# Kernel tuning notes

Hardware: AMD Instinct MI355X
Metric: run time of the kernel (lower is better)

## Reference

```python
import jax, jax.numpy as jnp
import numpy as np

N = 100000   # nodes
E = 3200000  # edges
F = 128      # in = hidden = out channels
V = 8        # virtual nodes
L = 3        # conv layers
EPS = 1e-5


def setup_inputs() -> dict:
    key = jax.random.key(0)
    ks = jax.random.split(key, 16)
    rn = lambda k, s, sc=0.05: jax.random.normal(k, s, jnp.float32) * sc
    return {
        "x": rn(ks[0], (N, F), 1.0),
        "edge_index": jax.random.randint(ks[1], (2, E), 0, N, jnp.int32),
        "vn_mask": jax.random.randint(ks[2], (V, N), 0, 2, jnp.int32).astype(bool),
        "Wc": rn(ks[3], (L, F, F)),
        "bc": rn(ks[4], (L, F)),
        "bn_g": jnp.ones((L, F), jnp.float32),
        "bn_b": jnp.zeros((L, F), jnp.float32),
        "vn_embed": rn(ks[5], (V, F)),
        "mlp_W1": rn(ks[6], (L - 1, V, F, 2 * F)),
        "mlp_b1": rn(ks[7], (L - 1, V, 2 * F)),
        "ln1_g": jnp.ones((L - 1, V, 2 * F), jnp.float32),
        "ln1_b": jnp.zeros((L - 1, V, 2 * F), jnp.float32),
        "mlp_W2": rn(ks[8], (L - 1, V, 2 * F, F)),
        "mlp_b2": rn(ks[9], (L - 1, V, F)),
        "ln2_g": jnp.ones((L - 1, V, F), jnp.float32),
        "ln2_b": jnp.zeros((L - 1, V, F), jnp.float32),
    }


def _ln(h, g, b):
    m = h.mean(-1, keepdims=True)
    v = ((h - m) ** 2).mean(-1, keepdims=True)
    return (h - m) * jax.lax.rsqrt(v + EPS) * g + b


def _bn(h, g, b):  # training-mode batch stats over nodes (dropout p=0)
    m = h.mean(0)
    v = ((h - m) ** 2).mean(0)
    return (h - m) * jax.lax.rsqrt(v + EPS) * g + b


def reference(x, edge_index, vn_mask, Wc, bc, bn_g, bn_b, vn_embed,
              mlp_W1, mlp_b1, ln1_g, ln1_b, mlp_W2, mlp_b2, ln2_g, ln2_b):
    src, dst = edge_index[0], edge_index[1]
    loops = jnp.arange(N, dtype=src.dtype)
    src_f = jnp.concatenate([src, loops])   # GCN adds self-loops
    dst_f = jnp.concatenate([dst, loops])
    deg = jax.ops.segment_sum(jnp.ones(src_f.shape[0], x.dtype), dst_f, num_segments=N)
    dinv = jnp.where(deg > 0, jax.lax.rsqrt(deg), 0.0)
    norm = dinv[src_f] * dinv[dst_f]        # sym-normalized edge weights

    def gcn(h, W, b):  # PyG GCNConv: linear -> normalized scatter-sum -> bias
        hl = h @ W
        out = jax.ops.segment_sum(hl[src_f] * norm[:, None], dst_f, num_segments=N)
        return out + b

    maskf = vn_mask.astype(x.dtype)  # [V, N]
    vn = vn_embed                    # [V, F]
    embs = [x]
    for layer in range(L):
        h = embs[layer] + vn.sum(0, keepdims=True)       # aggregation='sum'
        h = gcn(h, Wc[layer], bc[layer])
        h = _bn(h, bn_g[layer], bn_b[layer])
        if layer != L - 1:
            h = jax.nn.relu(h)
        embs.append(h)
        if layer < L - 1:
            pooled = maskf @ embs[layer]                 # per-VN global_add_pool
            tmp = pooled + vn
            h1 = jax.nn.relu(jnp.einsum('vf,vfh->vh', tmp, mlp_W1[layer]) + mlp_b1[layer])
            h1 = _ln(h1, ln1_g[layer], ln1_b[layer])
            h2 = jax.nn.relu(jnp.einsum('vh,vhf->vf', h1, mlp_W2[layer]) + mlp_b2[layer])
            vn = _ln(h2, ln2_g[layer], ln2_b[layer])
    return embs[-1]  # JK='last'
```

## Files before the change

kernel.cpp:

```cpp
#include <hip/hip_runtime.h>
#include <hip/hip_bf16.h>
#include <hip/hip_fp16.h>

#define NN 100000
#define EE 3200000
#define FF 128
#define F2 256
#define VV 8
#define LL 3
#define EPSV 1e-5f
#define NB 98

static inline int idiv(int a, int b){ return (a + b - 1) / b; }

__global__ void k_deg(const int* __restrict__ dst, int* __restrict__ edeg){
  int stride = gridDim.x * 256;
  for (int e = blockIdx.x * 256 + threadIdx.x; e < EE; e += stride)
    atomicAdd(&edeg[dst[e]], 1);
}

__global__ void k_scanA(const int* __restrict__ edeg, int* __restrict__ offs,
                        int* __restrict__ bsum, float* __restrict__ dinv){
  __shared__ int s[1024];
  int t = threadIdx.x;
  int i = blockIdx.x * 1024 + t;
  int v = (i < NN) ? edeg[i] : 0;
  if (i < NN) dinv[i] = rsqrtf((float)(v + 1));
  int x = v;
  s[t] = x; __syncthreads();
  for (int d = 1; d < 1024; d <<= 1){
    int y = (t >= d) ? s[t - d] : 0;
    __syncthreads();
    x += y; s[t] = x;
    __syncthreads();
  }
  if (i < NN) offs[i] = x - v;
  if (t == 1023) bsum[blockIdx.x] = x;
}

__global__ void k_scanB(int* __restrict__ bsum){
  __shared__ int s[128];
  int t = threadIdx.x;
  s[t] = (t < NB) ? bsum[t] : 0;
  __syncthreads();
  if (t == 0){
    int run = 0;
    for (int k = 0; k < NB; ++k){ int tmp = s[k]; s[k] = run; run += tmp; }
  }
  __syncthreads();
  if (t < NB) bsum[t] = s[t];
}

__global__ void k_scanC(int* __restrict__ offs, const int* __restrict__ bsum,
                        int* __restrict__ cursor){
  int i = blockIdx.x * 256 + threadIdx.x;
  if (i < NN){
    int o = offs[i] + bsum[i >> 10];
    offs[i] = o;
    cursor[i] = o;
  }
  if (i == 0) offs[NN] = EE;
}

__global__ void k_scatter(const int* __restrict__ src, const int* __restrict__ dst,
                          int* __restrict__ cursor, int* __restrict__ ssorted){
  int stride = gridDim.x * 256;
  for (int e = blockIdx.x * 256 + threadIdx.x; e < EE; e += stride){
    int d = dst[e];
    int pos = atomicAdd(&cursor[d], 1);
    ssorted[pos] = src[e];
  }
}

__global__ void k_maskdetect(const unsigned char* __restrict__ m, int* __restrict__ flag){
  int any = 0;
  for (int t = threadIdx.x; t < 4096; t += 256)
    if ((t & 3) && m[t]) any = 1;
  if (any) atomicOr(flag, 1);
}

__launch_bounds__(256)
__global__ void k_matmul(const float* __restrict__ in, const float* __restrict__ W,
                         const float* __restrict__ vn, const float* __restrict__ dinv,
                         uint2* __restrict__ hlb){
  __shared__ float Ws[FF * FF];
  __shared__ float As[8 * FF];
  __shared__ float vs[FF];
  __shared__ float rv[FF];
  int tid = threadIdx.x;
  for (int t = tid; t < FF * FF; t += 256) Ws[t] = W[t];
  if (tid < FF){
    float s = 0.f;
    for (int v = 0; v < VV; ++v) s += vn[v * FF + tid];
    vs[tid] = s;
  }
  __syncthreads();
  if (tid < FF){
    float a = 0.f;
    for (int k = 0; k < FF; ++k) a += vs[k] * Ws[k * FF + tid];
    rv[tid] = a;
  }
  __syncthreads();
  int row = tid >> 5;
  int col = (tid & 31) * 4;
  float4 rvv = *(const float4*)&rv[col];
  for (int base = blockIdx.x * 8; base < NN; base += gridDim.x * 8){
    for (int t = tid; t < 8 * FF; t += 256)
      As[t] = in[(base + (t >> 7)) * FF + (t & 127)];
    __syncthreads();
    float4 acc = rvv;
    #pragma unroll 8
    for (int k = 0; k < FF; ++k){
      float a = As[row * FF + k];
      float4 wv = *(const float4*)&Ws[k * FF + col];
      acc.x += a * wv.x; acc.y += a * wv.y; acc.z += a * wv.z; acc.w += a * wv.w;
    }
    float d = dinv[base + row];
    __half2 h01 = __floats2half2_rn(acc.x * d, acc.y * d);
    __half2 h23 = __floats2half2_rn(acc.z * d, acc.w * d);
    uint2 pk;
    pk.x = *reinterpret_cast<unsigned int*>(&h01);
    pk.y = *reinterpret_cast<unsigned int*>(&h23);
    hlb[(size_t)(base + row) * 32 + (tid & 31)] = pk;
    __syncthreads();
  }
}

__launch_bounds__(256)
__global__ void k_gather(const unsigned int* __restrict__ hlb, const float* __restrict__ dinv,
                         const int* __restrict__ offs, const int* __restrict__ ssorted,
                         float2* __restrict__ agg2, float* __restrict__ stats){
  int tid = threadIdx.x;
  int lane = tid & 63;
  int wid = (blockIdx.x * 256 + tid) >> 6;
  int nw = (gridDim.x * 256) >> 6;
  float s0 = 0.f, s1 = 0.f, q0 = 0.f, q1 = 0.f;
  for (int n = wid; n < NN; n += nw){
    int off0 = offs[n], off1 = offs[n + 1];
    unsigned int ps = hlb[(size_t)n * 64 + lane];
    float2 acc = __half22float2(*reinterpret_cast<__half2*>(&ps));
    #pragma unroll 4
    for (int e = off0; e < off1; ++e){
      unsigned int p = hlb[(size_t)ssorted[e] * 64 + lane];
      float2 f = __half22float2(*reinterpret_cast<__half2*>(&p));
      acc.x += f.x; acc.y += f.y;
    }
    float dv = dinv[n];
    float v0 = acc.x * dv, v1 = acc.y * dv;
    agg2[(size_t)n * 64 + lane] = make_float2(v0, v1);
    s0 += v0; s1 += v1; q0 += v0 * v0; q1 += v1 * v1;
  }
  __shared__ float4 red[256];
  red[tid] = make_float4(s0, s1, q0, q1);
  __syncthreads();
  if (tid < 64){
    float4 a = red[tid], b = red[tid + 64], c = red[tid + 128], d = red[tid + 192];
    a.x += b.x + c.x + d.x; a.y += b.y + c.y + d.y;
    a.z += b.z + c.z + d.z; a.w += b.w + c.w + d.w;
    atomicAdd(&stats[2 * tid], a.x);
    atomicAdd(&stats[2 * tid + 1], a.y);
    atomicAdd(&stats[FF + 2 * tid], a.z);
    atomicAdd(&stats[FF + 2 * tid + 1], a.w);
  }
}

__launch_bounds__(256)
__global__ void k_bnapply(float4* __restrict__ h, const float* __restrict__ stats,
                          const float* __restrict__ g, const float* __restrict__ b,
                          int relu){
  __shared__ float ss[2 * FF];
  int tid = threadIdx.x;
  if (tid < FF){
    float mean = stats[tid] * (1.0f / NN);
    float var  = stats[FF + tid] * (1.0f / NN) - mean * mean;
    float sc = rsqrtf(var + EPSV) * g[tid];
    ss[tid] = sc;
    ss[FF + tid] = b[tid] - mean * sc;
  }
  __syncthreads();
  int n4 = NN * FF / 4;
  int stride = gridDim.x * 256;
  for (int i = blockIdx.x * 256 + tid; i < n4; i += stride){
    int c = (i & 31) * 4;
    float4 v = h[i];
    float4 sc = *(const float4*)&ss[c];
    float4 sh = *(const float4*)&ss[FF + c];
    v.x = v.x * sc.x + sh.x;
    v.y = v.y * sc.y + sh.y;
    v.z = v.z * sc.z + sh.z;
    v.w = v.w * sc.w + sh.w;
    if (relu){
      v.x = fmaxf(v.x, 0.f); v.y = fmaxf(v.y, 0.f);
      v.z = fmaxf(v.z, 0.f); v.w = fmaxf(v.w, 0.f);
    }
    h[i] = v;
  }
}

__global__ void k_pool(const float* __restrict__ emb, const unsigned char* __restrict__ m8,
                       const int* __restrict__ m32, const int* __restrict__ flag,
                       float* __restrict__ pooled){
  int isb = *flag;
  int tid = blockIdx.x * 256 + threadIdx.x;
  int j = tid & 127;
  int r = tid >> 7;
  int rs = (gridDim.x * 256) >> 7;
  float acc[VV];
  #pragma unroll
  for (int v = 0; v < VV; ++v) acc[v] = 0.f;
  for (; r < NN; r += rs){
    float xv = emb[r * FF + j];
    #pragma unroll
    for (int v = 0; v < VV; ++v){
      int mv = isb ? (int)m8[v * NN + r] : m32[v * NN + r];
      if (mv) acc[v] += xv;
    }
  }
  #pragma unroll
  for (int v = 0; v < VV; ++v) atomicAdd(&pooled[v * FF + j], acc[v]);
}

__device__ __forceinline__ float blockSum(float x, float* red, int tid){
  red[tid] = x; __syncthreads();
  #pragma unroll
  for (int s = 128; s >= 1; s >>= 1){
    if (tid < s) red[tid] += red[tid + s];
    __syncthreads();
  }
  float r = red[0];
  __syncthreads();
  return r;
}

__launch_bounds__(256)
__global__ void k_vnmlp(const float* __restrict__ pooled, const float* __restrict__ vnin,
                        const float* __restrict__ W1, const float* __restrict__ b1,
                        const float* __restrict__ g1, const float* __restrict__ bb1,
                        const float* __restrict__ W2, const float* __restrict__ b2,
                        const float* __restrict__ g2, const float* __restrict__ bb2,
                        float* __restrict__ vnout){
  int v = blockIdx.x;
  int tid = threadIdx.x;
  __shared__ float tmp_s[FF];
  __shared__ float h1_s[F2];
  __shared__ float red[256];
  if (tid < FF) tmp_s[tid] = pooled[v * FF + tid] + vnin[v * FF + tid];
  __syncthreads();
  const float* W1v = W1 + (size_t)v * FF * F2;
  float acc = b1[v * F2 + tid];
  for (int k = 0; k < FF; ++k) acc += tmp_s[k] * W1v[k * F2 + tid];
  acc = fmaxf(acc, 0.f);
  float sum = blockSum(acc, red, tid);
  float sq  = blockSum(acc * acc, red, tid);
  float mean = sum * (1.f / F2);
  float var  = sq * (1.f / F2) - mean * mean;
  float y = (acc - mean) * rsqrtf(var + EPSV) * g1[v * F2 + tid] + bb1[v * F2 + tid];
  h1_s[tid] = y;
  __syncthreads();
  const float* W2v = W2 + (size_t)v * F2 * FF;
  float h2 = 0.f;
  if (tid < FF){
    float a2 = b2[v * FF + tid];
    for (int k = 0; k < F2; ++k) a2 += h1_s[k] * W2v[k * FF + tid];
    h2 = fmaxf(a2, 0.f);
  }
  float sum2 = blockSum((tid < FF) ? h2 : 0.f, red, tid);
  float sq2  = blockSum((tid < FF) ? h2 * h2 : 0.f, red, tid);
  float mean2 = sum2 * (1.f / FF);
  float var2  = sq2 * (1.f / FF) - mean2 * mean2;
  if (tid < FF)
    vnout[v * FF + tid] = (h2 - mean2) * rsqrtf(var2 + EPSV) * g2[v * FF + tid]
                          + bb2[v * FF + tid];
}

extern "C" void kernel_launch(void* const* d_in, const int* in_sizes, int n_in,
                              void* d_out, int out_size, void* d_ws, size_t ws_size,
                              hipStream_t stream){
  const float* x        = (const float*)d_in[0];
  const int*   ei       = (const int*)d_in[1];
  const unsigned char* vmask8 = (const unsigned char*)d_in[2];
  const int*   vmask32  = (const int*)d_in[2];
  const float* Wc       = (const float*)d_in[3];
  const float* bn_g     = (const float*)d_in[5];
  const float* bn_b     = (const float*)d_in[6];
  const float* vn_embed = (const float*)d_in[7];
  const float* mlp_W1   = (const float*)d_in[8];
  const float* mlp_b1   = (const float*)d_in[9];
  const float* ln1_g    = (const float*)d_in[10];
  const float* ln1_b    = (const float*)d_in[11];
  const float* mlp_W2   = (const float*)d_in[12];
  const float* mlp_b2   = (const float*)d_in[13];
  const float* ln2_g    = (const float*)d_in[14];
  const float* ln2_b    = (const float*)d_in[15];
  float* out = (float*)d_out;

  unsigned int* hlb = (unsigned int*)d_ws;
  float* bufB    = (float*)(hlb + (size_t)NN * 64);
  int*   ssorted = (int*)(bufB + (size_t)NN * FF);
  int*   offs    = ssorted + EE;
  int*   cursor  = offs + NN + 1;
  int*   edeg    = cursor + NN;
  int*   bsum    = edeg + NN;
  float* dinv    = (float*)(bsum + 128);
  float* stats   = dinv + NN;
  float* pooled  = stats + 2 * FF;
  float* vnA     = pooled + VV * FF;
  float* vnB     = vnA + VV * FF;
  int*   mflag   = (int*)(vnB + VV * FF);

  const int* esrc = ei;
  const int* edst = ei + EE;

  hipMemsetAsync(edeg, 0, NN * sizeof(int), stream);
  k_deg<<<1024, 256, 0, stream>>>(edst, edeg);
  k_scanA<<<NB, 1024, 0, stream>>>(edeg, offs, bsum, dinv);
  k_scanB<<<1, 128, 0, stream>>>(bsum);
  k_scanC<<<idiv(NN, 256), 256, 0, stream>>>(offs, bsum, cursor);
  k_scatter<<<2048, 256, 0, stream>>>(esrc, edst, cursor, ssorted);

  hipMemsetAsync(mflag, 0, sizeof(int), stream);
  k_maskdetect<<<1, 256, 0, stream>>>(vmask8, mflag);

  const float* vncur = vn_embed;
  const float* embin = x;
  float* vnbufs[2] = {vnA, vnB};

  for (int l = 0; l < LL; ++l){
    float* agg = (l == 0) ? bufB : out;
    const float* Wl = Wc + (size_t)l * FF * FF;

    k_matmul<<<2048, 256, 0, stream>>>(embin, Wl, vncur, dinv, (uint2*)hlb);

    if (l < LL - 1){
      hipMemsetAsync(pooled, 0, VV * FF * sizeof(float), stream);
      k_pool<<<1024, 256, 0, stream>>>(embin, vmask8, vmask32, mflag, pooled);
    }

    hipMemsetAsync(stats, 0, 2 * FF * sizeof(float), stream);
    k_gather<<<2048, 256, 0, stream>>>(hlb, dinv, offs, ssorted, (float2*)agg, stats);
    k_bnapply<<<1024, 256, 0, stream>>>((float4*)agg, stats,
                                        bn_g + l * FF, bn_b + l * FF, (l < LL - 1) ? 1 : 0);

    if (l < LL - 1){
      k_vnmlp<<<VV, 256, 0, stream>>>(pooled, vncur,
          mlp_W1 + (size_t)l * VV * FF * F2, mlp_b1 + (size_t)l * VV * F2,
          ln1_g + (size_t)l * VV * F2, ln1_b + (size_t)l * VV * F2,
          mlp_W2 + (size_t)l * VV * F2 * FF, mlp_b2 + (size_t)l * VV * FF,
          ln2_g + (size_t)l * VV * FF, ln2_b + (size_t)l * VV * FF,
          vnbufs[l]);
      vncur = vnbufs[l];
      embin = agg;
    }
  }
}
```

Measured before the change: 1.741 ms.

## Fold BN+ReLU into next layer loads and two-pass bucketed CSR build

The batch-norm scale/shift and ReLU are no longer applied in a separate in-place pass for the first two layers. A tiny kernel computes the per-channel scale and shift, and the next layer's matmul and pool kernels apply them while loading their inputs. The edge scatter is split into a coarse bucket pass keyed by dst>>5, which packs the dst low bits with src, and a per-bucket placement pass, to improve locality of the atomic cursor updates and writes. The gather unroll is also raised; this adds an extra pass over the edges and reuses the hlb buffer as scratch for binning.

```diff
diff --git a/kernel.cpp b/kernel.cpp
--- a/kernel.cpp
+++ b/kernel.cpp
@@ -10,6 +10,10 @@
 #define LL 3
 #define EPSV 1e-5f
 #define NB 98
+#define BSH 5
+#define NBKT 3125
+#define SRCBITS 17
+#define SRCMASK 0x1FFFF
 
 static inline int idiv(int a, int b){ return (a + b - 1) / b; }
 
@@ -62,13 +66,31 @@
   if (i == 0) offs[NN] = EE;
 }
 
-__global__ void k_scatter(const int* __restrict__ src, const int* __restrict__ dst,
-                          int* __restrict__ cursor, int* __restrict__ ssorted){
+__global__ void k_binit(const int* __restrict__ offs, int* __restrict__ bktcur){
+  int b = blockIdx.x * 256 + threadIdx.x;
+  if (b < NBKT) bktcur[b] = offs[b << BSH];
+}
+
+__global__ void k_bin(const int* __restrict__ src, const int* __restrict__ dst,
+                      int* __restrict__ bktcur, unsigned int* __restrict__ binned){
   int stride = gridDim.x * 256;
   for (int e = blockIdx.x * 256 + threadIdx.x; e < EE; e += stride){
     int d = dst[e];
+    int pos = atomicAdd(&bktcur[d >> BSH], 1);
+    binned[pos] = ((unsigned int)(d & 31) << SRCBITS) | (unsigned int)src[e];
+  }
+}
+
+__global__ void k_place(const unsigned int* __restrict__ binned, const int* __restrict__ offs,
+                        int* __restrict__ cursor, int* __restrict__ ssorted){
+  int b = blockIdx.x;
+  int e0 = offs[b << BSH];
+  int e1 = offs[(b + 1) << BSH];
+  for (int e = e0 + threadIdx.x; e < e1; e += 256){
+    unsigned int v = binned[e];
+    int d = (b << BSH) | (int)(v >> SRCBITS);
     int pos = atomicAdd(&cursor[d], 1);
-    ssorted[pos] = src[e];
+    ssorted[pos] = (int)(v & SRCMASK);
   }
 }
 
@@ -82,17 +104,21 @@
 __launch_bounds__(256)
 __global__ void k_matmul(const float* __restrict__ in, const float* __restrict__ W,
                          const float* __restrict__ vn, const float* __restrict__ dinv,
+                         const float* __restrict__ ss, int hasbn,
                          uint2* __restrict__ hlb){
   __shared__ float Ws[FF * FF];
   __shared__ float As[8 * FF];
   __shared__ float vs[FF];
   __shared__ float rv[FF];
+  __shared__ float scs[FF], shs[FF];
   int tid = threadIdx.x;
   for (int t = tid; t < FF * FF; t += 256) Ws[t] = W[t];
   if (tid < FF){
     float s = 0.f;
     for (int v = 0; v < VV; ++v) s += vn[v * FF + tid];
     vs[tid] = s;
+    scs[tid] = hasbn ? ss[tid] : 1.0f;
+    shs[tid] = hasbn ? ss[FF + tid] : 0.0f;
   }
   __syncthreads();
   if (tid < FF){
@@ -105,8 +131,17 @@
   int col = (tid & 31) * 4;
   float4 rvv = *(const float4*)&rv[col];
   for (int base = blockIdx.x * 8; base < NN; base += gridDim.x * 8){
-    for (int t = tid; t < 8 * FF; t += 256)
-      As[t] = in[(base + (t >> 7)) * FF + (t & 127)];
+    if (hasbn){
+      for (int t = tid; t < 8 * FF; t += 256){
+        int c = t & 127;
+        float v = in[(base + (t >> 7)) * FF + c];
+        v = fmaf(v, scs[c], shs[c]);
+        As[t] = fmaxf(v, 0.f);
+      }
+    } else {
+      for (int t = tid; t < 8 * FF; t += 256)
+        As[t] = in[(base + (t >> 7)) * FF + (t & 127)];
+    }
     __syncthreads();
     float4 acc = rvv;
     #pragma unroll 8
@@ -139,7 +174,7 @@
     int off0 = offs[n], off1 = offs[n + 1];
     unsigned int ps = hlb[(size_t)n * 64 + lane];
     float2 acc = __half22float2(*reinterpret_cast<__half2*>(&ps));
-    #pragma unroll 4
+    #pragma unroll 8
     for (int e = off0; e < off1; ++e){
       unsigned int p = hlb[(size_t)ssorted[e] * 64 + lane];
       float2 f = __half22float2(*reinterpret_cast<__half2*>(&p));
@@ -164,10 +199,19 @@
   }
 }
 
+__global__ void k_bnfin(const float* __restrict__ stats, const float* __restrict__ g,
+                        const float* __restrict__ b, float* __restrict__ ss){
+  int j = threadIdx.x;
+  float mean = stats[j] * (1.0f / NN);
+  float var  = stats[FF + j] * (1.0f / NN) - mean * mean;
+  float sc = rsqrtf(var + EPSV) * g[j];
+  ss[j] = sc;
+  ss[FF + j] = b[j] - mean * sc;
+}
+
 __launch_bounds__(256)
 __global__ void k_bnapply(float4* __restrict__ h, const float* __restrict__ stats,
-                          const float* __restrict__ g, const float* __restrict__ b,
-                          int relu){
+                          const float* __restrict__ g, const float* __restrict__ b){
   __shared__ float ss[2 * FF];
   int tid = threadIdx.x;
   if (tid < FF){
@@ -189,27 +233,28 @@
     v.y = v.y * sc.y + sh.y;
     v.z = v.z * sc.z + sh.z;
     v.w = v.w * sc.w + sh.w;
-    if (relu){
-      v.x = fmaxf(v.x, 0.f); v.y = fmaxf(v.y, 0.f);
-      v.z = fmaxf(v.z, 0.f); v.w = fmaxf(v.w, 0.f);
-    }
     h[i] = v;
   }
 }
 
 __global__ void k_pool(const float* __restrict__ emb, const unsigned char* __restrict__ m8,
                        const int* __restrict__ m32, const int* __restrict__ flag,
+                       const float* __restrict__ ss, int hasbn,
                        float* __restrict__ pooled){
   int isb = *flag;
   int tid = blockIdx.x * 256 + threadIdx.x;
   int j = tid & 127;
   int r = tid >> 7;
   int rs = (gridDim.x * 256) >> 7;
+  float sc = hasbn ? ss[j] : 1.0f;
+  float sh = hasbn ? ss[FF + j] : 0.0f;
   float acc[VV];
   #pragma unroll
   for (int v = 0; v < VV; ++v) acc[v] = 0.f;
   for (; r < NN; r += rs){
     float xv = emb[r * FF + j];
+    xv = fmaf(xv, sc, sh);
+    if (hasbn) xv = fmaxf(xv, 0.f);
     #pragma unroll
     for (int v = 0; v < VV; ++v){
       int mv = isb ? (int)m8[v * NN + r] : m32[v * NN + r];
@@ -295,15 +340,19 @@
   float* out = (float*)d_out;
 
   unsigned int* hlb = (unsigned int*)d_ws;
+  unsigned int* binned = hlb;
   float* bufB    = (float*)(hlb + (size_t)NN * 64);
   int*   ssorted = (int*)(bufB + (size_t)NN * FF);
   int*   offs    = ssorted + EE;
   int*   cursor  = offs + NN + 1;
   int*   edeg    = cursor + NN;
   int*   bsum    = edeg + NN;
-  float* dinv    = (float*)(bsum + 128);
+  int*   bktcur  = bsum + 128;
+  float* dinv    = (float*)(bktcur + NBKT);
   float* stats   = dinv + NN;
-  float* pooled  = stats + 2 * FF;
+  float* ssA     = stats + 2 * FF;
+  float* ssB     = ssA + 2 * FF;
+  float* pooled  = ssB + 2 * FF;
   float* vnA     = pooled + VV * FF;
   float* vnB     = vnA + VV * FF;
   int*   mflag   = (int*)(vnB + VV * FF);
@@ -316,32 +365,36 @@
   k_scanA<<<NB, 1024, 0, stream>>>(edeg, offs, bsum, dinv);
   k_scanB<<<1, 128, 0, stream>>>(bsum);
   k_scanC<<<idiv(NN, 256), 256, 0, stream>>>(offs, bsum, cursor);
-  k_scatter<<<2048, 256, 0, stream>>>(esrc, edst, cursor, ssorted);
+  k_binit<<<idiv(NBKT, 256), 256, 0, stream>>>(offs, bktcur);
+  k_bin<<<2048, 256, 0, stream>>>(esrc, edst, bktcur, binned);
+  k_place<<<NBKT, 256, 0, stream>>>(binned, offs, cursor, ssorted);
 
   hipMemsetAsync(mflag, 0, sizeof(int), stream);
   k_maskdetect<<<1, 256, 0, stream>>>(vmask8, mflag);
 
   const float* vncur = vn_embed;
   const float* embin = x;
+  float* ssbufs[2] = {ssA, ssB};
+  const float* sscur = nullptr;
   float* vnbufs[2] = {vnA, vnB};
 
   for (int l = 0; l < LL; ++l){
-    float* agg = (l == 0) ? bufB : out;
+    float* agg = (l < LL - 1) ? bufB : out;
     const float* Wl = Wc + (size_t)l * FF * FF;
-
-    k_matmul<<<2048, 256, 0, stream>>>(embin, Wl, vncur, dinv, (uint2*)hlb);
+    int hasbn = (l > 0) ? 1 : 0;
+
+    k_matmul<<<2048, 256, 0, stream>>>(embin, Wl, vncur, dinv, sscur, hasbn, (uint2*)hlb);
 
     if (l < LL - 1){
       hipMemsetAsync(pooled, 0, VV * FF * sizeof(float), stream);
-      k_pool<<<1024, 256, 0, stream>>>(embin, vmask8, vmask32, mflag, pooled);
+      k_pool<<<1024, 256, 0, stream>>>(embin, vmask8, vmask32, mflag, sscur, hasbn, pooled);
     }
 
     hipMemsetAsync(stats, 0, 2 * FF * sizeof(float), stream);
     k_gather<<<2048, 256, 0, stream>>>(hlb, dinv, offs, ssorted, (float2*)agg, stats);
-    k_bnapply<<<1024, 256, 0, stream>>>((float4*)agg, stats,
-                                        bn_g + l * FF, bn_b + l * FF, (l < LL - 1) ? 1 : 0);
 
     if (l < LL - 1){
+      k_bnfin<<<1, 128, 0, stream>>>(stats, bn_g + l * FF, bn_b + l * FF, ssbufs[l]);
       k_vnmlp<<<VV, 256, 0, stream>>>(pooled, vncur,
           mlp_W1 + (size_t)l * VV * FF * F2, mlp_b1 + (size_t)l * VV * F2,
           ln1_g + (size_t)l * VV * F2, ln1_b + (size_t)l * VV * F2,
@@ -349,7 +402,10 @@
           ln2_g + (size_t)l * VV * FF, ln2_b + (size_t)l * VV * FF,
           vnbufs[l]);
       vncur = vnbufs[l];
+      sscur = ssbufs[l];
       embin = agg;
-    }
-  }
-}
+    } else {
+      k_bnapply<<<1024, 256, 0, stream>>>((float4*)out, stats, bn_g + l * FF, bn_b + l * FF);
+    }
+  }
+}
```

Result: slower. 1.893 ms (+8.7%).
